# Kernel tuning notes

Measured on AMD Instinct MI355X. Metric: run time of the kernel, lower is better.

The kernel has to match this reference:

```python
import jax, jax.numpy as jnp
import numpy as np

T, S, F, A = 256, 256, 1024, 256


def setup_inputs() -> dict:
    key = jax.random.key(0)
    ks = jax.random.split(key, 7)
    scale = 0.02
    return {
        "batch_data": jax.random.normal(ks[0], (T * S, F), dtype=jnp.float32),
        "a_w": jax.random.normal(ks[1], (F, A), dtype=jnp.float32) * scale,
        "a_b": jax.random.normal(ks[2], (A,), dtype=jnp.float32) * scale,
        "b_w": jax.random.normal(ks[3], (F, A), dtype=jnp.float32) * scale,
        "b_b": jax.random.normal(ks[4], (A,), dtype=jnp.float32) * scale,
        "g_w": jax.random.normal(ks[5], (F, F), dtype=jnp.float32) * scale,
        "g_b": jax.random.normal(ks[6], (F,), dtype=jnp.float32) * scale,
        "s": S,
        "t": T,
    }


def reference(batch_data, a_w, a_b, b_w, b_b, g_w, g_b, s, t):
    # Linear projections then reshape to (t, s, dim)
    theta = (batch_data @ a_w + a_b).reshape(t, s, -1)   # (t, s, A)
    phi = (batch_data @ b_w + b_b).reshape(t, s, -1)     # (t, s, A)
    feats = (batch_data @ g_w + g_b).reshape(t, s, -1)   # (t, s, F)
    # Per-t bilinear attention: theta @ phi^T, no softmax
    attn = jnp.einsum("tsa,tra->tsr", theta, phi)        # (t, s, s)
    results = jnp.einsum("tsr,trf->tsf", attn, feats)    # (t, s, F)
    return results / (s + t)
```

## Files before the change

kernel.cpp:

```cpp
#include <hip/hip_runtime.h>
#include <stdint.h>

#define TT 256
#define SS 256
#define FF 1024
#define AA 256

typedef __attribute__((ext_vector_type(8))) short short8;
typedef __attribute__((ext_vector_type(4))) float floatx4;

__device__ __forceinline__ unsigned short f2bf(float f) {
  unsigned int u = __float_as_uint(f);
  u += 0x7FFFu + ((u >> 16) & 1u);
  return (unsigned short)(u >> 16);
}

__device__ __forceinline__ void gl_lds16(const unsigned short* g, unsigned short* l) {
  __builtin_amdgcn_global_load_lds(
      (__attribute__((address_space(1))) void*)(g),
      (__attribute__((address_space(3))) void*)(l), 16, 0, 0);
}

__global__ void k_transpose_cvt(const float* __restrict__ W,
                                unsigned short* __restrict__ WT,
                                int K, int N) {
  __shared__ float tile[32][33];
  const int bk = blockIdx.x * 32, bn = blockIdx.y * 32;
  const int tx = threadIdx.x, ty = threadIdx.y;
  for (int i = ty; i < 32; i += 8)
    tile[i][tx] = W[(size_t)(bk + i) * N + bn + tx];
  __syncthreads();
  for (int i = ty; i < 32; i += 8)
    WT[(size_t)(bn + i) * K + bk + tx] = f2bf(tile[tx][i]);
}

__global__ __launch_bounds__(256) void k_cvt(const float* __restrict__ in,
                                             unsigned short* __restrict__ out,
                                             unsigned int n8) {
  unsigned int i = blockIdx.x * 256u + threadIdx.x;
  const unsigned int stride = gridDim.x * 256u;
  for (; i < n8; i += stride) {
    const size_t base = (size_t)i * 8;
    const floatx4 v0 = *(const floatx4*)(in + base);
    const floatx4 v1 = *(const floatx4*)(in + base + 4);
    ushort4 h0, h1;
    h0.x = f2bf(v0.x); h0.y = f2bf(v0.y); h0.z = f2bf(v0.z); h0.w = f2bf(v0.w);
    h1.x = f2bf(v1.x); h1.y = f2bf(v1.y); h1.z = f2bf(v1.z); h1.w = f2bf(v1.w);
    *(ushort4*)(out + base) = h0;
    *(ushort4*)(out + base + 4) = h1;
  }
}

__device__ __forceinline__ void stage_half(const unsigned short* G,
                                           unsigned short* L, int tid) {
  const int wave = tid >> 6, lane = tid & 63;
#pragma unroll
  for (int c = 0; c < 2; ++c) {
    const int chunk = c * 8 + wave;
    const int r = chunk * 8 + (lane >> 3);
    const int k8 = (lane & 7) ^ (lane >> 3);
    gl_lds16(G + (size_t)r * FF + k8 * 8, L + chunk * 512);
  }
}

__device__ __forceinline__ short8 ldsfrag(const unsigned short* h, int row,
                                          int col) {
  return *(const short8*)&h[row * 64 + (col ^ ((row & 7) << 3))];
}

__global__ __launch_bounds__(512, 2) void k_proj3(
    const unsigned short* __restrict__ batchH,
    const unsigned short* __restrict__ aT,
    const unsigned short* __restrict__ bT,
    const unsigned short* __restrict__ gT,
    const float* __restrict__ a_b, const float* __restrict__ b_b,
    const float* __restrict__ g_b,
    unsigned short* __restrict__ theta,
    unsigned short* __restrict__ phi,
    unsigned short* __restrict__ featsT,
    int mbase) {
  __shared__ unsigned short lds[65536];
  unsigned short* As = lds;
  unsigned short* Bs = lds + 32768;

  const int nwg = gridDim.x;
  const int hb = blockIdx.x;
  const int logical = (hb & 7) * (nwg >> 3) + (hb >> 3);
  const int nt = logical % 6;
  const int mtile = logical / 6;
  const int m0l = mtile * 256;
  const int m0 = mbase + m0l;

  const unsigned short* Wt; const float* bias; int nb0, mode;
  if (nt == 0)      { Wt = aT; bias = a_b; nb0 = 0;              mode = 0; }
  else if (nt == 1) { Wt = bT; bias = b_b; nb0 = 0;              mode = 1; }
  else              { Wt = gT; bias = g_b; nb0 = (nt - 2) * 256; mode = 2; }

  const int tid = threadIdx.x;
  const int wave = tid >> 6, lane = tid & 63;
  const int wm = wave >> 2, wn = wave & 3;
  const int lr = lane & 15, lq = lane >> 4;
  const int brow = (wn & 1) * 64;

  const unsigned short* Ap = batchH + (size_t)m0l * FF;
  const unsigned short* Bp = Wt + (size_t)nb0 * FF;

  floatx4 acc[8][4];
#pragma unroll
  for (int i = 0; i < 8; i++)
#pragma unroll
    for (int j = 0; j < 4; j++) acc[i][j] = (floatx4)0.0f;

  stage_half(Bp,                 Bs + 0 * 8192, tid);
  stage_half(Bp + 128 * FF,      Bs + 1 * 8192, tid);
  stage_half(Ap,                 As + 0 * 8192, tid);
  stage_half(Ap + 128 * FF,      As + 1 * 8192, tid);
  stage_half(Bp + 64,            Bs + 2 * 8192, tid);
  stage_half(Bp + 128 * FF + 64, Bs + 3 * 8192, tid);

  short8 af0[4][2], af1[4][2], bf[4][2];
  const int NKT = FF / 64;

#pragma unroll 1
  for (int kt = 0; kt < NKT; ++kt) {
    const unsigned short* Ah = As + ((kt & 1) * 2 + wm) * 8192;
    const unsigned short* Bh = Bs + ((kt & 1) * 2 + (wn >> 1)) * 8192;
    const int nbuf = 1 - (kt & 1);

    if (kt + 1 < NKT) {
      stage_half(Ap + (size_t)(kt + 1) * 64, As + (nbuf * 2 + 0) * 8192, tid);
      asm volatile("s_waitcnt vmcnt(6)" ::: "memory");
    } else {
      asm volatile("s_waitcnt vmcnt(0)" ::: "memory");
    }
    asm volatile("s_barrier" ::: "memory");
#pragma unroll
    for (int i = 0; i < 4; ++i)
#pragma unroll
      for (int ks = 0; ks < 2; ++ks)
        af0[i][ks] = ldsfrag(Ah, i * 16 + lr, ks * 32 + lq * 8);
#pragma unroll
    for (int j = 0; j < 2; ++j)
#pragma unroll
      for (int ks = 0; ks < 2; ++ks)
        bf[j][ks] = ldsfrag(Bh, brow + j * 16 + lr, ks * 32 + lq * 8);
#pragma unroll
    for (int j = 2; j < 4; ++j)
#pragma unroll
      for (int ks = 0; ks < 2; ++ks)
        bf[j][ks] = ldsfrag(Bh, brow + j * 16 + lr, ks * 32 + lq * 8);
    __builtin_amdgcn_s_setprio(1);
#pragma unroll
    for (int i = 0; i < 4; ++i)
#pragma unroll
      for (int j = 0; j < 2; ++j)
#pragma unroll
        for (int ks = 0; ks < 2; ++ks)
          acc[i][j] = __builtin_amdgcn_mfma_f32_16x16x32_bf16(
              af0[i][ks], bf[j][ks], acc[i][j], 0, 0, 0);
    __builtin_amdgcn_s_setprio(0);
    asm volatile("s_barrier" ::: "memory");

    if (kt + 1 < NKT)
      stage_half(Ap + 128 * FF + (size_t)(kt + 1) * 64,
                 As + (nbuf * 2 + 1) * 8192, tid);
#pragma unroll
    for (int i = 0; i < 4; ++i)
#pragma unroll
      for (int ks = 0; ks < 2; ++ks)
        af1[i][ks] = ldsfrag(Ah, 64 + i * 16 + lr, ks * 32 + lq * 8);
    __builtin_amdgcn_s_setprio(1);
#pragma unroll
    for (int i = 0; i < 4; ++i)
#pragma unroll
      for (int j = 0; j < 2; ++j)
#pragma unroll
        for (int ks = 0; ks < 2; ++ks)
          acc[i][2 + j] = __builtin_amdgcn_mfma_f32_16x16x32_bf16(
              af0[i][ks], bf[2 + j][ks], acc[i][2 + j], 0, 0, 0);
    __builtin_amdgcn_s_setprio(0);
    asm volatile("s_barrier" ::: "memory");

    if (kt + 2 < NKT)
      stage_half(Bp + (size_t)(kt + 2) * 64, Bs + ((kt & 1) * 2 + 0) * 8192,
                 tid);
    __builtin_amdgcn_s_setprio(1);
#pragma unroll
    for (int i = 0; i < 4; ++i)
#pragma unroll
      for (int j = 0; j < 2; ++j)
#pragma unroll
        for (int ks = 0; ks < 2; ++ks)
          acc[4 + i][j] = __builtin_amdgcn_mfma_f32_16x16x32_bf16(
              af1[i][ks], bf[j][ks], acc[4 + i][j], 0, 0, 0);
    __builtin_amdgcn_s_setprio(0);
    asm volatile("s_barrier" ::: "memory");

    if (kt + 2 < NKT)
      stage_half(Bp + 128 * FF + (size_t)(kt + 2) * 64,
                 Bs + ((kt & 1) * 2 + 1) * 8192, tid);
    __builtin_amdgcn_s_setprio(1);
#pragma unroll
    for (int i = 0; i < 4; ++i)
#pragma unroll
      for (int j = 0; j < 2; ++j)
#pragma unroll
        for (int ks = 0; ks < 2; ++ks)
          acc[4 + i][2 + j] = __builtin_amdgcn_mfma_f32_16x16x32_bf16(
              af1[i][ks], bf[2 + j][ks], acc[4 + i][2 + j], 0, 0, 0);
    __builtin_amdgcn_s_setprio(0);
    asm volatile("s_barrier" ::: "memory");
  }

#pragma unroll
  for (int fi = 0; fi < 8; ++fi) {
    const int srow = wm * 128 + fi * 16 + lq * 4;
#pragma unroll
    for (int j = 0; j < 4; ++j) {
      const int col = wn * 64 + j * 16 + lr;
      const float bv = bias[nb0 + col];
      if (mode == 2) {
        const int t = m0 >> 8;
        ushort4 h;
        h.x = f2bf(acc[fi][j][0] + bv);
        h.y = f2bf(acc[fi][j][1] + bv);
        h.z = f2bf(acc[fi][j][2] + bv);
        h.w = f2bf(acc[fi][j][3] + bv);
        *(ushort4*)&featsT[((size_t)t * FF + nb0 + col) * SS + srow] = h;
      } else {
        unsigned short* outp = (mode == 0) ? theta : phi;
#pragma unroll
        for (int rr = 0; rr < 4; ++rr)
          outp[(size_t)(m0 + srow + rr) * AA + col] = f2bf(acc[fi][j][rr] + bv);
      }
    }
  }
}

template <bool OUTF32>
__global__ __launch_bounds__(256) void k_gemm_bt(
    const unsigned short* __restrict__ A, const unsigned short* __restrict__ B,
    void* __restrict__ C, int N, int K, long sA, long sB, long sC,
    float scale) {
  __shared__ unsigned short As[128 * 32];
  __shared__ unsigned short Bs[128 * 32];

  const unsigned gx = gridDim.x, gy = gridDim.y;
  unsigned h = (blockIdx.z * gy + blockIdx.y) * gx + blockIdx.x;
  const unsigned nwg = gx * gy * gridDim.z;
  unsigned l = (nwg & 7) ? h : (h & 7) * (nwg >> 3) + (h >> 3);
  const unsigned bx = l % gx; l /= gx;
  const unsigned by = l % gy; const unsigned bz = l / gy;

  const unsigned short* Ab = A + (size_t)bz * sA;
  const unsigned short* Bb = B + (size_t)bz * sB;
  const int n0 = bx * 128, m0 = by * 128;
  const int tid = threadIdx.x, lane = tid & 63, wave = tid >> 6;
  const int wm = wave >> 1, wn = wave & 1, lr = lane & 15, lq = lane >> 4;

  floatx4 acc[4][4];
#pragma unroll
  for (int i = 0; i < 4; i++)
#pragma unroll
    for (int j = 0; j < 4; j++) acc[i][j] = (floatx4)0.0f;

  for (int k0 = 0; k0 < K; k0 += 32) {
    __syncthreads();
    int sl = tid;
    gl_lds16(Ab + (size_t)(m0 + (sl >> 2)) * K + k0 + (sl & 3) * 8,
             &As[wave * 512]);
    gl_lds16(Bb + (size_t)(n0 + (sl >> 2)) * K + k0 + (sl & 3) * 8,
             &Bs[wave * 512]);
    sl = tid + 256;
    gl_lds16(Ab + (size_t)(m0 + (sl >> 2)) * K + k0 + (sl & 3) * 8,
             &As[2048 + wave * 512]);
    gl_lds16(Bb + (size_t)(n0 + (sl >> 2)) * K + k0 + (sl & 3) * 8,
             &Bs[2048 + wave * 512]);
    __syncthreads();

    short8 af[4], bfr[4];
#pragma unroll
    for (int i = 0; i < 4; i++)
      af[i] = *(const short8*)&As[(wm * 64 + i * 16 + lr) * 32 + lq * 8];
#pragma unroll
    for (int j = 0; j < 4; j++)
      bfr[j] = *(const short8*)&Bs[(wn * 64 + j * 16 + lr) * 32 + lq * 8];
#pragma unroll
    for (int i = 0; i < 4; i++)
#pragma unroll
      for (int j = 0; j < 4; j++)
        acc[i][j] = __builtin_amdgcn_mfma_f32_16x16x32_bf16(af[i], bfr[j],
                                                            acc[i][j], 0, 0, 0);
  }

#pragma unroll
  for (int i = 0; i < 4; i++) {
    const int row0 = wm * 64 + i * 16 + lq * 4;
#pragma unroll
    for (int j = 0; j < 4; j++) {
      const int col = wn * 64 + j * 16 + lr;
#pragma unroll
      for (int rr = 0; rr < 4; rr++) {
        const float v = acc[i][j][rr] * scale;
        if (OUTF32) {
          float* Cb = (float*)C + (size_t)bz * sC;
          Cb[(size_t)(m0 + row0 + rr) * N + n0 + col] = v;
        } else {
          unsigned short* Cb = (unsigned short*)C + (size_t)bz * sC;
          Cb[(size_t)(m0 + row0 + rr) * N + n0 + col] = f2bf(v);
        }
      }
    }
  }
}

extern "C" void kernel_launch(void* const* d_in, const int* in_sizes, int n_in,
                              void* d_out, int out_size, void* d_ws,
                              size_t ws_size, hipStream_t stream) {
  const float* batch = (const float*)d_in[0];
  const float* a_w   = (const float*)d_in[1];
  const float* a_b   = (const float*)d_in[2];
  const float* b_w   = (const float*)d_in[3];
  const float* b_b   = (const float*)d_in[4];
  const float* g_w   = (const float*)d_in[5];
  const float* g_b   = (const float*)d_in[6];
  float* out = (float*)d_out;

  unsigned short* ws     = (unsigned short*)d_ws;
  unsigned short* aT     = ws;
  unsigned short* bT     = aT + (size_t)AA * FF;
  unsigned short* gT     = bT + (size_t)AA * FF;
  unsigned short* theta  = gT + (size_t)FF * FF;
  unsigned short* phi    = theta + (size_t)TT * SS * AA;
  unsigned short* featsT = phi + (size_t)TT * SS * AA;
  unsigned short* attn   = featsT + (size_t)TT * FF * SS;

  dim3 tb(32, 8);
  k_transpose_cvt<<<dim3(32, 8),  tb, 0, stream>>>(a_w, aT, FF, AA);
  k_transpose_cvt<<<dim3(32, 8),  tb, 0, stream>>>(b_w, bT, FF, AA);
  k_transpose_cvt<<<dim3(32, 32), tb, 0, stream>>>(g_w, gT, FF, FF);

  const size_t base_bytes  = 238026752ull;
  const size_t batch_bytes = (size_t)TT * SS * FF * 2;
  if (ws_size >= base_bytes + batch_bytes) {
    unsigned short* batchH = attn + (size_t)TT * SS * SS;
    k_cvt<<<2048, 256, 0, stream>>>(batch, batchH,
                                    (unsigned int)((size_t)TT * SS * FF / 8));
    k_proj3<<<6 * 256, 512, 0, stream>>>(batchH, aT, bT, gT, a_b, b_b, g_b,
                                         theta, phi, featsT, 0);
  } else {
    unsigned short* batchH = attn;
    const int CHUNK_ROWS = 16384;
    for (int c = 0; c < 4; c++) {
      const float* src = batch + (size_t)c * CHUNK_ROWS * FF;
      k_cvt<<<2048, 256, 0, stream>>>(
          src, batchH, (unsigned int)((size_t)CHUNK_ROWS * FF / 8));
      k_proj3<<<6 * 64, 512, 0, stream>>>(batchH, aT, bT, gT, a_b, b_b, g_b,
                                          theta, phi, featsT, c * CHUNK_ROWS);
    }
  }

  k_gemm_bt<false><<<dim3(2, 2, TT), 256, 0, stream>>>(
      theta, phi, attn, SS, AA, (long)SS * AA, (long)SS * AA, (long)SS * SS,
      1.0f);

  k_gemm_bt<true><<<dim3(8, 2, TT), 256, 0, stream>>>(
      attn, featsT, out, FF, SS, (long)SS * SS, (long)FF * SS, (long)SS * FF,
      1.0f / 512.0f);
}
```

Before: 435.8 us.

## Software-pipeline LDS fragment loads behind MFMA phases in projection GEMM

Restructures the GEMM main loop so LDS fragment reads for the next phase (and the next k-tile's first fragments) are issued after each MFMA block, overlapping LDS latency with matrix math. Wait counts and barriers are reshuffled to match the new staging order, including a prologue that preloads the first fragments. This adds extra barriers and more live registers, and depends on the vmcnt bookkeeping being correct.

```diff
diff --git a/kernel.cpp b/kernel.cpp
--- a/kernel.cpp
+++ b/kernel.cpp
@@ -121,34 +121,34 @@
   short8 af0[4][2], af1[4][2], bf[4][2];
   const int NKT = FF / 64;
 
+  asm volatile("s_waitcnt vmcnt(4)" ::: "memory");
+  asm volatile("s_barrier" ::: "memory");
+  {
+    const unsigned short* Ah0 = As + wm * 8192;
+    const unsigned short* Bh0 = Bs + (wn >> 1) * 8192;
+#pragma unroll
+    for (int i = 0; i < 4; ++i)
+#pragma unroll
+      for (int ks = 0; ks < 2; ++ks)
+        af0[i][ks] = ldsfrag(Ah0, i * 16 + lr, ks * 32 + lq * 8);
+#pragma unroll
+    for (int j = 0; j < 2; ++j)
+#pragma unroll
+      for (int ks = 0; ks < 2; ++ks)
+        bf[j][ks] = ldsfrag(Bh0, brow + j * 16 + lr, ks * 32 + lq * 8);
+  }
+
 #pragma unroll 1
   for (int kt = 0; kt < NKT; ++kt) {
     const unsigned short* Ah = As + ((kt & 1) * 2 + wm) * 8192;
     const unsigned short* Bh = Bs + ((kt & 1) * 2 + (wn >> 1)) * 8192;
     const int nbuf = 1 - (kt & 1);
-
-    if (kt + 1 < NKT) {
+    const unsigned short* Ah2 = As + (nbuf * 2 + wm) * 8192;
+    const unsigned short* Bh2 = Bs + (nbuf * 2 + (wn >> 1)) * 8192;
+
+    if (kt + 1 < NKT)
       stage_half(Ap + (size_t)(kt + 1) * 64, As + (nbuf * 2 + 0) * 8192, tid);
-      asm volatile("s_waitcnt vmcnt(6)" ::: "memory");
-    } else {
-      asm volatile("s_waitcnt vmcnt(0)" ::: "memory");
-    }
-    asm volatile("s_barrier" ::: "memory");
-#pragma unroll
-    for (int i = 0; i < 4; ++i)
-#pragma unroll
-      for (int ks = 0; ks < 2; ++ks)
-        af0[i][ks] = ldsfrag(Ah, i * 16 + lr, ks * 32 + lq * 8);
-#pragma unroll
-    for (int j = 0; j < 2; ++j)
-#pragma unroll
-      for (int ks = 0; ks < 2; ++ks)
-        bf[j][ks] = ldsfrag(Bh, brow + j * 16 + lr, ks * 32 + lq * 8);
-#pragma unroll
-    for (int j = 2; j < 4; ++j)
-#pragma unroll
-      for (int ks = 0; ks < 2; ++ks)
-        bf[j][ks] = ldsfrag(Bh, brow + j * 16 + lr, ks * 32 + lq * 8);
+    asm volatile("s_barrier" ::: "memory");
     __builtin_amdgcn_s_setprio(1);
 #pragma unroll
     for (int i = 0; i < 4; ++i)
@@ -159,16 +159,21 @@
           acc[i][j] = __builtin_amdgcn_mfma_f32_16x16x32_bf16(
               af0[i][ks], bf[j][ks], acc[i][j], 0, 0, 0);
     __builtin_amdgcn_s_setprio(0);
-    asm volatile("s_barrier" ::: "memory");
-
-    if (kt + 1 < NKT)
+#pragma unroll
+    for (int j = 2; j < 4; ++j)
+#pragma unroll
+      for (int ks = 0; ks < 2; ++ks)
+        bf[j][ks] = ldsfrag(Bh, brow + j * 16 + lr, ks * 32 + lq * 8);
+    asm volatile("s_barrier" ::: "memory");
+
+    if (kt + 1 < NKT) {
       stage_half(Ap + 128 * FF + (size_t)(kt + 1) * 64,
                  As + (nbuf * 2 + 1) * 8192, tid);
-#pragma unroll
-    for (int i = 0; i < 4; ++i)
-#pragma unroll
-      for (int ks = 0; ks < 2; ++ks)
-        af1[i][ks] = ldsfrag(Ah, 64 + i * 16 + lr, ks * 32 + lq * 8);
+      asm volatile("s_waitcnt vmcnt(8)" ::: "memory");
+    } else {
+      asm volatile("s_waitcnt vmcnt(0)" ::: "memory");
+    }
+    asm volatile("s_barrier" ::: "memory");
     __builtin_amdgcn_s_setprio(1);
 #pragma unroll
     for (int i = 0; i < 4; ++i)
@@ -179,11 +184,17 @@
           acc[i][2 + j] = __builtin_amdgcn_mfma_f32_16x16x32_bf16(
               af0[i][ks], bf[2 + j][ks], acc[i][2 + j], 0, 0, 0);
     __builtin_amdgcn_s_setprio(0);
+#pragma unroll
+    for (int i = 0; i < 4; ++i)
+#pragma unroll
+      for (int ks = 0; ks < 2; ++ks)
+        af1[i][ks] = ldsfrag(Ah, 64 + i * 16 + lr, ks * 32 + lq * 8);
     asm volatile("s_barrier" ::: "memory");
 
     if (kt + 2 < NKT)
       stage_half(Bp + (size_t)(kt + 2) * 64, Bs + ((kt & 1) * 2 + 0) * 8192,
                  tid);
+    asm volatile("s_barrier" ::: "memory");
     __builtin_amdgcn_s_setprio(1);
 #pragma unroll
     for (int i = 0; i < 4; ++i)
@@ -199,6 +210,11 @@
     if (kt + 2 < NKT)
       stage_half(Bp + 128 * FF + (size_t)(kt + 2) * 64,
                  Bs + ((kt & 1) * 2 + 1) * 8192, tid);
+    if (kt + 1 < NKT) {
+      if (kt + 2 < NKT) asm volatile("s_waitcnt vmcnt(4)" ::: "memory");
+      else              asm volatile("s_waitcnt vmcnt(0)" ::: "memory");
+    }
+    asm volatile("s_barrier" ::: "memory");
     __builtin_amdgcn_s_setprio(1);
 #pragma unroll
     for (int i = 0; i < 4; ++i)
@@ -209,6 +225,18 @@
           acc[4 + i][2 + j] = __builtin_amdgcn_mfma_f32_16x16x32_bf16(
               af1[i][ks], bf[2 + j][ks], acc[4 + i][2 + j], 0, 0, 0);
     __builtin_amdgcn_s_setprio(0);
+    if (kt + 1 < NKT) {
+#pragma unroll
+      for (int i = 0; i < 4; ++i)
+#pragma unroll
+        for (int ks = 0; ks < 2; ++ks)
+          af0[i][ks] = ldsfrag(Ah2, i * 16 + lr, ks * 32 + lq * 8);
+#pragma unroll
+      for (int j = 0; j < 2; ++j)
+#pragma unroll
+        for (int ks = 0; ks < 2; ++ks)
+          bf[j][ks] = ldsfrag(Bh2, brow + j * 16 + lr, ks * 32 + lq * 8);
+    }
     asm volatile("s_barrier" ::: "memory");
   }
 
```

Result: slower. 445.3 us (+2.2%).
